# Optimization experiments

Hardware: AMD Instinct MI355X
Metric: run time of the kernel (lower is better)

## Reference

```python
import jax, jax.numpy as jnp
import numpy as np

B, T, C = 4, 2048, 1024
N_HEAD = 16
HEAD_DIM = C // N_HEAD


def setup_inputs() -> dict:
    key = jax.random.key(0)
    k1, k2, k3 = jax.random.split(key, 3)
    x = jax.random.normal(k1, (B, T, C), dtype=jnp.float32)
    # w_attn corresponds to c_attn.weight.T (shape [C, 3C]); w_proj to c_proj.weight.T ([C, C])
    w_attn = jax.random.normal(k2, (C, 3 * C), dtype=jnp.float32) * (1.0 / np.sqrt(C))
    w_proj = jax.random.normal(k3, (C, C), dtype=jnp.float32) * (1.0 / np.sqrt(C))
    return {"x": x, "w_attn": w_attn, "w_proj": w_proj}


def reference(x, w_attn, w_proj):
    Bv, Tv, Cv = x.shape
    qkv = x @ w_attn                                  # [B, T, 3C]
    q, k, v = jnp.split(qkv, 3, axis=-1)
    # [B, T, C] -> [B, H, T, Dh]
    def heads(t):
        return t.reshape(Bv, Tv, N_HEAD, HEAD_DIM).transpose(0, 2, 1, 3)
    q, k, v = heads(q), heads(k), heads(v)
    scale = 1.0 / np.sqrt(HEAD_DIM)
    att = jnp.einsum('bhqd,bhkd->bhqk', q, k) * scale   # [B, H, T, T]
    causal = jnp.tril(jnp.ones((Tv, Tv), dtype=bool))
    att = jnp.where(causal[None, None, :, :], att, -jnp.inf)
    att = jax.nn.softmax(att, axis=-1)
    y = jnp.einsum('bhqk,bhkd->bhqd', att, v)            # [B, H, T, Dh]
    y = y.transpose(0, 2, 1, 3).reshape(Bv, Tv, Cv)      # [B, T, C]
    y = y @ w_proj
    # present_kv = (k, v); return main output y plus cache, matching torch module
    return y, (k, v)
```

## Files before the change

### kernel.cpp

```cpp
#include <hip/hip_runtime.h>

#define B_  4
#define T_  2048
#define C_  1024
#define NH_ 16
#define DH_ 64

typedef __attribute__((ext_vector_type(8))) short bf16x8;
typedef __attribute__((ext_vector_type(4))) float f32x4;

__device__ __forceinline__ unsigned short f2bf(float f) {
  unsigned u = __builtin_bit_cast(unsigned, f);
  u += 0x7fffu + ((u >> 16) & 1u);
  return (unsigned short)(u >> 16);
}

__device__ __forceinline__ void gld16(const void* g, void* l) {
  __builtin_amdgcn_global_load_lds(
      (const __attribute__((address_space(1))) void*)g,
      (__attribute__((address_space(3))) void*)l, 16, 0, 0);
}

__global__ void k_cvt(const float* __restrict__ x, unsigned short* __restrict__ o, int n) {
  int i = (blockIdx.x * 256 + threadIdx.x) * 4;
  if (i < n) {
    const float4 v = *reinterpret_cast<const float4*>(x + i);
    ushort4 u;
    u.x = f2bf(v.x); u.y = f2bf(v.y); u.z = f2bf(v.z); u.w = f2bf(v.w);
    *reinterpret_cast<ushort4*>(o + i) = u;
  }
}

__global__ void k_transpose(const float* __restrict__ w, unsigned short* __restrict__ wt,
                            int K, int N) {
  __shared__ float tile[32][33];
  int tx = threadIdx.x, ty = threadIdx.y;
  int n0 = blockIdx.x * 32, k0 = blockIdx.y * 32;
  #pragma unroll
  for (int j = 0; j < 32; j += 8)
    tile[ty + j][tx] = w[(size_t)(k0 + ty + j) * N + n0 + tx];
  __syncthreads();
  #pragma unroll
  for (int j = 0; j < 32; j += 8)
    wt[(size_t)(n0 + ty + j) * K + k0 + tx] = f2bf(tile[tx][ty + j]);
}

template <int EPI>
__global__ __launch_bounds__(256, 2)
void k_gemm(const unsigned short* __restrict__ A,
            const unsigned short* __restrict__ Bt,
            int M, int N, int K,
            float* __restrict__ outF,
            unsigned short* __restrict__ qb,
            unsigned short* __restrict__ kb,
            unsigned short* __restrict__ vbT,
            float* __restrict__ kout,
            float* __restrict__ vout) {
  __shared__ __align__(16) unsigned short As[128 * 64];
  __shared__ __align__(16) unsigned short Bs[128 * 64];

  const int tid  = threadIdx.x;
  const int wave = tid >> 6;
  const int lane = tid & 63;
  const int l15  = lane & 15;
  const int quad = lane >> 4;
  const int wm   = (wave >> 1) * 64;
  const int wn   = (wave & 1) * 64;

  const int m0 = blockIdx.y * 128;
  const int n0 = blockIdx.x * 128;

  f32x4 acc[4][4];
  #pragma unroll
  for (int i = 0; i < 4; i++)
    #pragma unroll
    for (int j = 0; j < 4; j++)
      acc[i][j] = f32x4{0.f, 0.f, 0.f, 0.f};

  for (int k0 = 0; k0 < K; k0 += 64) {
    __syncthreads();
    #pragma unroll
    for (int i = 0; i < 4; i++) {
      int c0  = (wave * 4 + i) * 64;
      int c   = c0 + lane;
      int row = c >> 3, kc = c & 7;
      gld16(A  + (size_t)(m0 + row) * K + k0 + kc * 8, &As[c0 * 8]);
      gld16(Bt + (size_t)(n0 + row) * K + k0 + kc * 8, &Bs[c0 * 8]);
    }
    __syncthreads();

    bf16x8 af[4][2], bfr[4][2];
    #pragma unroll
    for (int mt = 0; mt < 4; mt++)
      #pragma unroll
      for (int kf = 0; kf < 2; kf++) {
        af[mt][kf]  = *reinterpret_cast<const bf16x8*>(&As[(wm + mt * 16 + l15) * 64 + kf * 32 + quad * 8]);
        bfr[mt][kf] = *reinterpret_cast<const bf16x8*>(&Bs[(wn + mt * 16 + l15) * 64 + kf * 32 + quad * 8]);
      }
    #pragma unroll
    for (int mt = 0; mt < 4; mt++)
      #pragma unroll
      for (int nt = 0; nt < 4; nt++)
        #pragma unroll
        for (int kf = 0; kf < 2; kf++)
          acc[mt][nt] = __builtin_amdgcn_mfma_f32_16x16x32_bf16(af[mt][kf], bfr[nt][kf], acc[mt][nt], 0, 0, 0);
  }

  #pragma unroll
  for (int mt = 0; mt < 4; mt++) {
    #pragma unroll
    for (int nt = 0; nt < 4; nt++) {
      #pragma unroll
      for (int r = 0; r < 4; r++) {
        float v  = acc[mt][nt][r];
        int   gm = m0 + wm + mt * 16 + quad * 4 + r;
        int   gn = n0 + wn + nt * 16 + l15;
        if constexpr (EPI == 1) {
          outF[(size_t)gm * N + gn] = v;
        } else {
          int b = gm >> 11, t = gm & 2047;
          int sec = gn >> 10, cn = gn & 1023;
          int h = cn >> 6, d = cn & 63;
          size_t idxN = (((size_t)(b * NH_ + h)) * T_ + t) * DH_ + d;
          size_t idxT = (((size_t)(b * NH_ + h)) * DH_ + d) * T_ + t;
          unsigned short bv = f2bf(v);
          if (sec == 0) { qb[idxN] = bv; }
          else if (sec == 1) { kb[idxN] = bv; kout[idxN] = v; }
          else { vbT[idxT] = bv; vout[idxN] = v; }
        }
      }
    }
  }
}

__global__ __launch_bounds__(256, 3)
void k_attn(const unsigned short* __restrict__ qb,
            const unsigned short* __restrict__ kb,
            const unsigned short* __restrict__ vbT,
            unsigned short* __restrict__ ya) {
  __shared__ __align__(16) unsigned short Ks[64 * 64];
  __shared__ __align__(16) unsigned short Vts[64 * 64];
  const int PLD = 72;
  __shared__ __align__(16) unsigned short Ps[4][16 * PLD];

  const int tid  = threadIdx.x;
  const int wave = tid >> 6;
  const int lane = tid & 63;
  const int l15  = lane & 15;
  const int quad = lane >> 4;

  const int blk  = blockIdx.x;
  const int pair = blk & 15;
  const int bh   = blk >> 4;
  const int q0p[2] = {pair * 64, (31 - pair) * 64};
  const int nkt[2] = {pair + 1, 32 - pair};
  const size_t base  = (size_t)bh * T_ * DH_;
  const size_t baseT = (size_t)bh * DH_ * T_;

  const float CS = 0.180336880f;
  const float PB = 17.3123404907f;

  bf16x8 qf[2][2];
  #pragma unroll
  for (int p = 0; p < 2; p++)
    #pragma unroll
    for (int kf = 0; kf < 2; kf++)
      qf[p][kf] = *reinterpret_cast<const bf16x8*>(
          qb + base + (size_t)(q0p[p] + wave * 16 + l15) * DH_ + kf * 32 + quad * 8);

  bf16x8 onesb;
  #pragma unroll
  for (int j = 0; j < 8; j++) onesb[j] = (short)0x3F80;

  f32x4 of[2][4], ls[2];
  #pragma unroll
  for (int p = 0; p < 2; p++) {
    ls[p] = f32x4{0.f, 0.f, 0.f, 0.f};
    #pragma unroll
    for (int nt = 0; nt < 4; nt++)
      of[p][nt] = f32x4{0.f, 0.f, 0.f, 0.f};
  }

  for (int kt = 0; kt < nkt[1]; kt++) {
    __syncthreads();
    #pragma unroll
    for (int i = 0; i < 2; i++) {
      int c0 = (wave * 2 + i) * 64;
      int c  = c0 + lane;
      gld16(kb + base + (size_t)kt * 4096 + (size_t)c * 8, &Ks[c0 * 8]);
      int row = c >> 3, col = c & 7;
      gld16(vbT + baseT + (size_t)row * T_ + kt * 64 + col * 8, &Vts[c0 * 8]);
    }
    __syncthreads();

    bf16x8 bk[4][2], vbf[4][2];
    #pragma unroll
    for (int nt = 0; nt < 4; nt++)
      #pragma unroll
      for (int kf = 0; kf < 2; kf++) {
        bk[nt][kf]  = *reinterpret_cast<const bf16x8*>(&Ks[(nt * 16 + l15) * 64 + kf * 32 + quad * 8]);
        vbf[nt][kf] = *reinterpret_cast<const bf16x8*>(&Vts[(nt * 16 + l15) * 64 + kf * 32 + quad * 8]);
      }

    #pragma unroll
    for (int p = 0; p < 2; p++) {
      if (kt >= nkt[p]) continue;

      f32x4 s[4];
      #pragma unroll
      for (int nt = 0; nt < 4; nt++) s[nt] = f32x4{0.f, 0.f, 0.f, 0.f};
      #pragma unroll
      for (int nt = 0; nt < 4; nt++)
        #pragma unroll
        for (int kf = 0; kf < 2; kf++)
          s[nt] = __builtin_amdgcn_mfma_f32_16x16x32_bf16(qf[p][kf], bk[nt][kf], s[nt], 0, 0, 0);

      if (kt == nkt[p] - 1) {
        #pragma unroll
        for (int nt = 0; nt < 4; nt++) {
          int gk = kt * 64 + nt * 16 + l15;
          #pragma unroll
          for (int r = 0; r < 4; r++) {
            int gq = q0p[p] + wave * 16 + quad * 4 + r;
            s[nt][r] = (gk <= gq) ? s[nt][r] : -3e38f;
          }
        }
      }

      #pragma unroll
      for (int nt = 0; nt < 4; nt++)
        #pragma unroll
        for (int r = 0; r < 4; r++) {
          float pv = __builtin_amdgcn_exp2f(__builtin_fmaf(s[nt][r], CS, -PB));
          Ps[wave][(quad * 4 + r) * PLD + nt * 16 + l15] = f2bf(pv);
        }

      bf16x8 pa[2];
      #pragma unroll
      for (int kf = 0; kf < 2; kf++)
        pa[kf] = *reinterpret_cast<const bf16x8*>(&Ps[wave][l15 * PLD + kf * 32 + quad * 8]);
      #pragma unroll
      for (int nt = 0; nt < 4; nt++)
        #pragma unroll
        for (int kf = 0; kf < 2; kf++)
          of[p][nt] = __builtin_amdgcn_mfma_f32_16x16x32_bf16(pa[kf], vbf[nt][kf], of[p][nt], 0, 0, 0);
      #pragma unroll
      for (int kf = 0; kf < 2; kf++)
        ls[p] = __builtin_amdgcn_mfma_f32_16x16x32_bf16(pa[kf], onesb, ls[p], 0, 0, 0);
    }
  }

  const int b = bh >> 4, h = bh & 15;
  #pragma unroll
  for (int p = 0; p < 2; p++)
    #pragma unroll
    for (int r = 0; r < 4; r++) {
      int t = q0p[p] + wave * 16 + quad * 4 + r;
      float inv = 1.f / ls[p][r];
      #pragma unroll
      for (int nt = 0; nt < 4; nt++) {
        int col = h * DH_ + nt * 16 + l15;
        ya[((size_t)(b * T_ + t)) * C_ + col] = f2bf(of[p][nt][r] * inv);
      }
    }
}

extern "C" void kernel_launch(void* const* d_in, const int* in_sizes, int n_in,
                              void* d_out, int out_size, void* d_ws, size_t ws_size,
                              hipStream_t stream) {
  const float* x      = (const float*)d_in[0];
  const float* w_attn = (const float*)d_in[1];
  const float* w_proj = (const float*)d_in[2];

  float* y    = (float*)d_out;
  float* kout = y + (size_t)B_ * T_ * C_;
  float* vout = kout + (size_t)B_ * T_ * C_;

  char* ws = (char*)d_ws;
  const size_t xe = (size_t)B_ * T_ * C_;
  unsigned short* xb  = (unsigned short*)ws;  ws += xe * 2;
  unsigned short* wab = (unsigned short*)ws;  ws += (size_t)3 * C_ * C_ * 2;
  unsigned short* wpb = (unsigned short*)ws;  ws += (size_t)C_ * C_ * 2;
  unsigned short* qbb = (unsigned short*)ws;  ws += xe * 2;
  unsigned short* kbb = (unsigned short*)ws;  ws += xe * 2;
  unsigned short* vbb = (unsigned short*)ws;  ws += xe * 2;
  unsigned short* ya  = xb;

  const int M = B_ * T_;

  k_cvt<<<(int)(xe / 4 / 256), 256, 0, stream>>>(x, xb, (int)xe);
  k_transpose<<<dim3(3 * C_ / 32, C_ / 32), dim3(32, 8), 0, stream>>>(w_attn, wab, C_, 3 * C_);
  k_transpose<<<dim3(C_ / 32, C_ / 32), dim3(32, 8), 0, stream>>>(w_proj, wpb, C_, C_);

  k_gemm<0><<<dim3(3 * C_ / 128, M / 128), 256, 0, stream>>>(
      xb, wab, M, 3 * C_, C_, nullptr, qbb, kbb, vbb, kout, vout);

  k_attn<<<dim3(B_ * NH_ * 16), 256, 0, stream>>>(qbb, kbb, vbb, ya);

  k_gemm<1><<<dim3(C_ / 128, M / 128), 256, 0, stream>>>(
      ya, wpb, M, C_, C_, y, nullptr, nullptr, nullptr, nullptr, nullptr);
}
```

Baseline: 351.8 us.

## Double-buffer GEMM LDS tiles with prefetch, XOR swizzle, and finer waitcnt barriers

Restructures the GEMM main loop to double-buffer the A and B tiles in LDS, split into two 32-wide K halves. The next tile is prefetched via global_load_lds while MFMAs run on the current one, and the loop waits only on partial vmcnt. It also XOR-swizzles the LDS layout to reduce bank conflicts and raises wave priority around the MFMA block. This is meant to hide global load latency and remove the two full syncthreads per K step, at the cost of doubled LDS use, which may lower occupancy.

```diff
diff --git a/kernel.cpp b/kernel.cpp
--- a/kernel.cpp
+++ b/kernel.cpp
@@ -56,8 +56,8 @@
             unsigned short* __restrict__ vbT,
             float* __restrict__ kout,
             float* __restrict__ vout) {
-  __shared__ __align__(16) unsigned short As[128 * 64];
-  __shared__ __align__(16) unsigned short Bs[128 * 64];
+  __shared__ __align__(16) unsigned short As[2][2][128 * 32];
+  __shared__ __align__(16) unsigned short Bs[2][2][128 * 32];
 
   const int tid  = threadIdx.x;
   const int wave = tid >> 6;
@@ -66,6 +66,7 @@
   const int quad = lane >> 4;
   const int wm   = (wave >> 1) * 64;
   const int wn   = (wave & 1) * 64;
+  const int swz  = (quad ^ (l15 & 3)) * 8;
 
   const int m0 = blockIdx.y * 128;
   const int n0 = blockIdx.x * 128;
@@ -77,33 +78,57 @@
     for (int j = 0; j < 4; j++)
       acc[i][j] = f32x4{0.f, 0.f, 0.f, 0.f};
 
-  for (int k0 = 0; k0 < K; k0 += 64) {
-    __syncthreads();
-    #pragma unroll
-    for (int i = 0; i < 4; i++) {
-      int c0  = (wave * 4 + i) * 64;
+  auto stage = [&](int kt, int h) {
+    unsigned short* da = &As[kt & 1][h][0];
+    unsigned short* db = &Bs[kt & 1][h][0];
+    const int kbase = kt * 64 + h * 32;
+    #pragma unroll
+    for (int i = 0; i < 2; i++) {
+      int c0  = (wave * 2 + i) * 64;
       int c   = c0 + lane;
-      int row = c >> 3, kc = c & 7;
-      gld16(A  + (size_t)(m0 + row) * K + k0 + kc * 8, &As[c0 * 8]);
-      gld16(Bt + (size_t)(n0 + row) * K + k0 + kc * 8, &Bs[c0 * 8]);
-    }
-    __syncthreads();
-
-    bf16x8 af[4][2], bfr[4][2];
-    #pragma unroll
-    for (int mt = 0; mt < 4; mt++)
-      #pragma unroll
-      for (int kf = 0; kf < 2; kf++) {
-        af[mt][kf]  = *reinterpret_cast<const bf16x8*>(&As[(wm + mt * 16 + l15) * 64 + kf * 32 + quad * 8]);
-        bfr[mt][kf] = *reinterpret_cast<const bf16x8*>(&Bs[(wn + mt * 16 + l15) * 64 + kf * 32 + quad * 8]);
-      }
-    #pragma unroll
-    for (int mt = 0; mt < 4; mt++)
-      #pragma unroll
-      for (int nt = 0; nt < 4; nt++)
-        #pragma unroll
-        for (int kf = 0; kf < 2; kf++)
-          acc[mt][nt] = __builtin_amdgcn_mfma_f32_16x16x32_bf16(af[mt][kf], bfr[nt][kf], acc[mt][nt], 0, 0, 0);
+      int row = c >> 2;
+      int sch = (c & 3) ^ (row & 3);
+      gld16(A  + (size_t)(m0 + row) * K + kbase + sch * 8, da + c0 * 8);
+      gld16(Bt + (size_t)(n0 + row) * K + kbase + sch * 8, db + c0 * 8);
+    }
+  };
+
+  const int NT = K >> 6;
+
+  stage(0, 0);
+  stage(0, 1);
+  asm volatile("s_waitcnt vmcnt(4)" ::: "memory");
+  __builtin_amdgcn_s_barrier();
+  __builtin_amdgcn_sched_barrier(0);
+
+  for (int t = 0; t < NT; ++t) {
+    const bool pre = (t + 1 < NT);
+    #pragma unroll
+    for (int h = 0; h < 2; ++h) {
+      if (pre) stage(t + 1, h);
+
+      const unsigned short* Au = &As[t & 1][h][0];
+      const unsigned short* Bu = &Bs[t & 1][h][0];
+      bf16x8 af[4], bfr[4];
+      #pragma unroll
+      for (int mt = 0; mt < 4; mt++) {
+        af[mt]  = *reinterpret_cast<const bf16x8*>(&Au[(wm + mt * 16 + l15) * 32 + swz]);
+        bfr[mt] = *reinterpret_cast<const bf16x8*>(&Bu[(wn + mt * 16 + l15) * 32 + swz]);
+      }
+
+      __builtin_amdgcn_s_setprio(1);
+      #pragma unroll
+      for (int mt = 0; mt < 4; mt++)
+        #pragma unroll
+        for (int nt = 0; nt < 4; nt++)
+          acc[mt][nt] = __builtin_amdgcn_mfma_f32_16x16x32_bf16(af[mt], bfr[nt], acc[mt][nt], 0, 0, 0);
+      __builtin_amdgcn_s_setprio(0);
+
+      if (pre) { asm volatile("s_waitcnt vmcnt(4)" ::: "memory"); }
+      else     { asm volatile("s_waitcnt vmcnt(0)" ::: "memory"); }
+      __builtin_amdgcn_s_barrier();
+      __builtin_amdgcn_sched_barrier(0);
+    }
   }
 
   #pragma unroll
@@ -118,11 +143,11 @@
         if constexpr (EPI == 1) {
           outF[(size_t)gm * N + gn] = v;
         } else {
-          int b = gm >> 11, t = gm & 2047;
+          int b = gm >> 11, t2 = gm & 2047;
           int sec = gn >> 10, cn = gn & 1023;
-          int h = cn >> 6, d = cn & 63;
-          size_t idxN = (((size_t)(b * NH_ + h)) * T_ + t) * DH_ + d;
-          size_t idxT = (((size_t)(b * NH_ + h)) * DH_ + d) * T_ + t;
+          int h2 = cn >> 6, d = cn & 63;
+          size_t idxN = (((size_t)(b * NH_ + h2)) * T_ + t2) * DH_ + d;
+          size_t idxT = (((size_t)(b * NH_ + h2)) * DH_ + d) * T_ + t2;
           unsigned short bv = f2bf(v);
           if (sec == 0) { qb[idxN] = bv; }
           else if (sec == 1) { kb[idxN] = bv; kout[idxN] = v; }
```

Result: slower. 368.9 us (+4.9%).
